# Kernel optimization log

Hardware: AMD Instinct MI355X
Metric: run time of the kernel (lower is better)

Reference implementation:

```python
import jax, jax.numpy as jnp
import numpy as np

D = 2048; Nl = 2; Nh = 32; Nkv = 8; V = 32000; Dh = 5632; Lm = 4096
B = 1; L = 2048; E = 1e-5
DHEAD = D // Nh  # 64


def setup_inputs() -> dict:
    key = jax.random.key(0)
    ks = jax.random.split(key, 10)
    s = 0.02
    rn = lambda k, shape: jax.random.normal(k, shape, jnp.float32) * s
    emb = rn(ks[0], (V, D))
    wq = rn(ks[1], (Nl, D, D))
    wk = rn(ks[2], (Nl, D, D * Nkv // Nh))
    wv = rn(ks[3], (Nl, D, D * Nkv // Nh))
    wa = rn(ks[4], (Nl, D, D))
    wg = rn(ks[5], (Nl, D, Dh))
    wu = rn(ks[6], (Nl, D, Dh))
    wd = rn(ks[7], (Nl, Dh, D))
    w_an = jnp.ones((Nl, D), jnp.float32)
    w_fn = jnp.ones((Nl, D), jnp.float32)
    w_on = jnp.ones((D,), jnp.float32)
    w_out = rn(ks[8], (D, V))
    # RoPE tables (interleaved-pair convention, matching reshape(..., -1, 2))
    theta = 1.0 / (10000.0 ** (jnp.arange(0, DHEAD, 2, dtype=jnp.float32) / DHEAD))
    freqs = jnp.outer(jnp.arange(Lm, dtype=jnp.float32), theta)  # [Lm, DHEAD//2]
    cos = jnp.cos(freqs)
    sin = jnp.sin(freqs)
    ti = jax.random.randint(ks[9], (B, L), 0, V)
    return dict(ti=ti, emb=emb, wq=wq, wk=wk, wv=wv, wa=wa, w_an=w_an, w_fn=w_fn,
                wg=wg, wu=wu, wd=wd, w_on=w_on, w_out=w_out, cos=cos, sin=sin)


def _rmsnorm(x, w):
    return x * jax.lax.rsqrt(jnp.mean(x * x, -1, keepdims=True) + E) * w


def _rope(x, cos, sin):
    # x: [B, L, H, DHEAD]; cos/sin: [1, L, 1, DHEAD//2]; interleaved pairs
    xs = x.reshape(*x.shape[:-1], DHEAD // 2, 2)
    xr, xi = xs[..., 0], xs[..., 1]
    r1 = xr * cos - xi * sin
    i1 = xr * sin + xi * cos
    return jnp.stack([r1, i1], axis=-1).reshape(x.shape)


def reference(ti, emb, wq, wk, wv, wa, w_an, w_fn, wg, wu, wd, w_on, w_out, cos, sin):
    cos_l = cos[:L].reshape(1, L, 1, DHEAD // 2)
    sin_l = sin[:L].reshape(1, L, 1, DHEAD // 2)
    mask = jnp.triu(jnp.full((1, 1, L, L), -jnp.inf, jnp.float32), 1)
    scale = 1.0 / jnp.sqrt(jnp.float32(DHEAD))
    rep = Nh // Nkv
    x = emb[ti]  # [B, L, D]
    for l in range(Nl):
        h = _rmsnorm(x, w_an[l])
        q = (h @ wq[l]).reshape(B, L, Nh, DHEAD)
        k = (h @ wk[l]).reshape(B, L, Nkv, DHEAD)
        v = (h @ wv[l]).reshape(B, L, Nkv, DHEAD)
        q = _rope(q, cos_l, sin_l)
        k = _rope(k, cos_l, sin_l)
        kx = jnp.repeat(k, rep, axis=2)  # GQA expand -> [B, L, Nh, DHEAD]
        vx = jnp.repeat(v, rep, axis=2)
        a = jnp.einsum('blhd,bmhd->bhlm', q, kx) * scale
        p = jax.nn.softmax(a + mask, axis=-1)
        sa = jnp.einsum('bhlm,bmhd->blhd', p, vx).reshape(B, L, D)
        x = x + sa @ wa[l]
        hf = _rmsnorm(x, w_fn[l])
        x = x + (jax.nn.silu(hf @ wg[l]) * (hf @ wu[l])) @ wd[l]
    return _rmsnorm(x, w_on) @ w_out  # [B, L, V]
```

## Files before the change

### kernel.cpp

```cpp
#include <hip/hip_runtime.h>
#include <hip/hip_bf16.h>

#define DMODEL 2048
#define LSEQ   2048
#define NHEAD  32
#define NKVH   8
#define DHEAD  64
#define DFF    5632
#define VOCAB  32000

typedef __attribute__((ext_vector_type(8))) short bf16x8;
typedef __attribute__((ext_vector_type(4))) float f32x4;
typedef __attribute__((ext_vector_type(8))) unsigned short ushort8;

__device__ __forceinline__ void gload_lds16(const __hip_bfloat16* g, __hip_bfloat16* l) {
  __builtin_amdgcn_global_load_lds((const void __attribute__((address_space(1)))*)g,
                                   (void __attribute__((address_space(3)))*)l, 16, 0, 0);
}

__device__ __forceinline__ float bfbits2f(unsigned short u) {
  return __uint_as_float(((unsigned int)u) << 16);
}
__device__ __forceinline__ unsigned short f2bfbits(float f) {
  unsigned int x = __float_as_uint(f);
  return (unsigned short)((x + 0x7fffu + ((x >> 16) & 1u)) >> 16);
}

__global__ __launch_bounds__(256) void embed_k(const int* __restrict__ ti,
                                               const float* __restrict__ emb,
                                               float* __restrict__ x) {
  const int row = blockIdx.x;
  const int t = threadIdx.x;
  const int tok = ti[row];
  const float4* s = (const float4*)(emb + (size_t)tok * DMODEL);
  float4* d = (float4*)(x + (size_t)row * DMODEL);
  d[t] = s[t];
  d[t + 256] = s[t + 256];
}

__global__ __launch_bounds__(256) void rmsnorm_k(const float* __restrict__ x,
                                                 const float* __restrict__ w,
                                                 __hip_bfloat16* __restrict__ out) {
  const int row = blockIdx.x;
  const int t = threadIdx.x;
  const float4* xr = (const float4*)(x + (size_t)row * DMODEL);
  float4 a = xr[t];
  float4 b = xr[t + 256];
  float ss = a.x*a.x + a.y*a.y + a.z*a.z + a.w*a.w
           + b.x*b.x + b.y*b.y + b.z*b.z + b.w*b.w;
  #pragma unroll
  for (int m = 32; m >= 1; m >>= 1) ss += __shfl_xor(ss, m);
  __shared__ float red[4];
  if ((t & 63) == 0) red[t >> 6] = ss;
  __syncthreads();
  const float tot = red[0] + red[1] + red[2] + red[3];
  const float sc = rsqrtf(tot * (1.0f / DMODEL) + 1e-5f);
  const float4* w4 = (const float4*)w;
  float4 wa_ = w4[t], wb_ = w4[t + 256];
  __hip_bfloat16* o = out + (size_t)row * DMODEL;
  o[4*t + 0] = __float2bfloat16(a.x * sc * wa_.x);
  o[4*t + 1] = __float2bfloat16(a.y * sc * wa_.y);
  o[4*t + 2] = __float2bfloat16(a.z * sc * wa_.z);
  o[4*t + 3] = __float2bfloat16(a.w * sc * wa_.w);
  o[1024 + 4*t + 0] = __float2bfloat16(b.x * sc * wb_.x);
  o[1024 + 4*t + 1] = __float2bfloat16(b.y * sc * wb_.y);
  o[1024 + 4*t + 2] = __float2bfloat16(b.z * sc * wb_.z);
  o[1024 + 4*t + 3] = __float2bfloat16(b.w * sc * wb_.w);
}

__global__ __launch_bounds__(256) void transpose_k(const float* __restrict__ src,
                                                   __hip_bfloat16* __restrict__ dst,
                                                   int K, int N, int rstride, int roff) {
  __shared__ float tile[64 * 65];
  const int kb = blockIdx.x * 64;
  const int nb = blockIdx.y * 64;
  const int t = threadIdx.x;
  #pragma unroll
  for (int i = 0; i < 16; ++i) {
    const int idx = t + 256 * i;
    const int r = idx >> 6, c = idx & 63;
    tile[r * 65 + c] = src[(size_t)(kb + r) * N + nb + c];
  }
  __syncthreads();
  #pragma unroll
  for (int i = 0; i < 16; ++i) {
    const int idx = t + 256 * i;
    const int n = idx >> 6, k = idx & 63;
    dst[((size_t)(nb + n) * rstride + roff) * K + kb + k] = __float2bfloat16(tile[k * 65 + n]);
  }
}

template <int EPI>
__global__ __launch_bounds__(256) void gemm_bt(const __hip_bfloat16* __restrict__ A,
                                               const __hip_bfloat16* __restrict__ Bt,
                                               float* __restrict__ Cf,
                                               __hip_bfloat16* __restrict__ Cb,
                                               int M, int N, int K) {
  __shared__ __align__(16) __hip_bfloat16 As[128 * 32];
  __shared__ __align__(16) __hip_bfloat16 Bs[128 * 32];
  const int tid = threadIdx.x;
  const int wave = tid >> 6;
  const int lane = tid & 63;
  const int nbx = M >> 7;
  const int nwg = nbx * (N >> 7);
  const int orig = blockIdx.y * nbx + blockIdx.x;
  const int wid = (orig & 7) * (nwg >> 3) + (orig >> 3);
  const int tm = (wid % nbx) << 7;
  const int tn = (wid / nbx) << 7;
  const int wr = (wave >> 1) * 64;
  const int wc = (wave & 1) * 64;
  const int fr = lane & 15;
  const int fg = lane >> 4;
  const f32x4 fzero = {0.f, 0.f, 0.f, 0.f};
  f32x4 acc[4][4];
  #pragma unroll
  for (int i = 0; i < 4; ++i)
    #pragma unroll
    for (int j = 0; j < 4; ++j) acc[i][j] = fzero;
  const int srow = wave * 32 + (lane >> 2);
  const int scol = (lane & 3) * 8;
  const __hip_bfloat16* gA = A + (size_t)(tm + srow) * K + scol;
  const __hip_bfloat16* gB = Bt + (size_t)(tn + srow) * K + scol;
  __hip_bfloat16* lA = &As[wave * 1024];
  __hip_bfloat16* lB = &Bs[wave * 1024];
  for (int k0 = 0; k0 < K; k0 += 32) {
    gload_lds16(gA, lA);
    gload_lds16(gA + (size_t)16 * K, lA + 512);
    gload_lds16(gB, lB);
    gload_lds16(gB + (size_t)16 * K, lB + 512);
    gA += 32; gB += 32;
    __syncthreads();
    bf16x8 af[4], bfr[4];
    #pragma unroll
    for (int i = 0; i < 4; ++i) af[i] = *(const bf16x8*)&As[(wr + i * 16 + fr) * 32 + fg * 8];
    #pragma unroll
    for (int j = 0; j < 4; ++j) bfr[j] = *(const bf16x8*)&Bs[(wc + j * 16 + fr) * 32 + fg * 8];
    #pragma unroll
    for (int i = 0; i < 4; ++i)
      #pragma unroll
      for (int j = 0; j < 4; ++j)
        acc[i][j] = __builtin_amdgcn_mfma_f32_16x16x32_bf16(af[i], bfr[j], acc[i][j], 0, 0, 0);
    __syncthreads();
  }
  #pragma unroll
  for (int i = 0; i < 4; ++i)
    #pragma unroll
    for (int j = 0; j < 4; ++j)
      #pragma unroll
      for (int r = 0; r < 4; ++r) {
        const int row = tm + wr + i * 16 + fg * 4 + r;
        const int col = tn + wc + j * 16 + fr;
        const float v = acc[i][j][r];
        if (EPI == 0) Cf[(size_t)row * N + col] = v;
        else if (EPI == 1) Cb[(size_t)row * N + col] = __float2bfloat16(v);
        else Cf[(size_t)row * N + col] += v;
      }
}

template <int EPI>
__global__ __launch_bounds__(512, 2) void gemm8p(const __hip_bfloat16* __restrict__ A,
                                                 const __hip_bfloat16* __restrict__ Bt,
                                                 float* __restrict__ Cf,
                                                 __hip_bfloat16* __restrict__ Cb,
                                                 int M, int N, int K) {
  __shared__ __align__(16) __hip_bfloat16 lds[2][2][256 * 64];
  const int tid = threadIdx.x;
  const int wave = tid >> 6;
  const int lane = tid & 63;
  const int nbx = M >> 8;
  const int nwg = nbx * (N >> 8);
  const int orig = blockIdx.y * nbx + blockIdx.x;
  const int wid = (orig & 7) * (nwg >> 3) + (orig >> 3);
  const int tm = (wid % nbx) << 8;
  const int tn = (wid / nbx) << 8;
  const int wm = wave >> 2;
  const int wn = wave & 3;
  const int fr = lane & 15;
  const int fg = lane >> 4;
  const int l3 = lane >> 3;
  const int l7 = lane & 7;
  const int swzcol = (l3 ^ l7) << 3;
  const size_t sK = (size_t)K;

  const __hip_bfloat16* pA = A + (size_t)(tm + wave * 8 + l3) * sK + swzcol;
  const __hip_bfloat16* pB = Bt + (size_t)(tn + wave * 8 + l3) * sK + swzcol;

  #pragma unroll
  for (int j = 0; j < 4; ++j) {
    gload_lds16(pA + (size_t)(j * 64) * sK, &lds[0][0][(j * 64 + wave * 8) * 64]);
    gload_lds16(pB + (size_t)(j * 64) * sK, &lds[0][1][(j * 64 + wave * 8) * 64]);
  }
  pA += 64; pB += 64;
  #pragma unroll
  for (int j = 0; j < 4; ++j) {
    gload_lds16(pA + (size_t)(j * 64) * sK, &lds[1][0][(j * 64 + wave * 8) * 64]);
    gload_lds16(pB + (size_t)(j * 64) * sK, &lds[1][1][(j * 64 + wave * 8) * 64]);
  }
  pA += 64; pB += 64;

  const f32x4 fzero = {0.f, 0.f, 0.f, 0.f};
  f32x4 acc[8][4];
  #pragma unroll
  for (int i = 0; i < 8; ++i)
    #pragma unroll
    for (int j = 0; j < 4; ++j) acc[i][j] = fzero;

  const int wmo = wm * 128;
  const int wno = wn * 64;
  const int rswz = (fr & 7) << 4;
  const int ct0 = ((fg * 16) ^ rswz) >> 1;
  const int ct1 = ((64 + fg * 16) ^ rswz) >> 1;

  asm volatile("s_waitcnt vmcnt(8)" ::: "memory");
  __builtin_amdgcn_s_barrier();
  __builtin_amdgcn_sched_barrier(0);

  const int NT = K >> 6;
  for (int kt = 0; kt < NT; ++kt) {
    const int cur = kt & 1;
    const __hip_bfloat16* LA = &lds[cur][0][0];
    const __hip_bfloat16* LB = &lds[cur][1][0];
    bf16x8 av[8][2], bv[4][2];
    #pragma unroll
    for (int mi = 0; mi < 8; ++mi) {
      av[mi][0] = *(const bf16x8*)&LA[(wmo + mi * 16 + fr) * 64 + ct0];
      av[mi][1] = *(const bf16x8*)&LA[(wmo + mi * 16 + fr) * 64 + ct1];
    }
    #pragma unroll
    for (int ni = 0; ni < 4; ++ni) {
      bv[ni][0] = *(const bf16x8*)&LB[(wno + ni * 16 + fr) * 64 + ct0];
      bv[ni][1] = *(const bf16x8*)&LB[(wno + ni * 16 + fr) * 64 + ct1];
    }
    asm volatile("s_waitcnt lgkmcnt(0)" ::: "memory");
    __builtin_amdgcn_sched_barrier(0);
    __builtin_amdgcn_s_barrier();
    __builtin_amdgcn_sched_barrier(0);
    const bool pre = (kt + 2 < NT);
    #pragma unroll
    for (int q = 0; q < 4; ++q) {
      if (pre) {
        gload_lds16(pA + (size_t)(q * 64) * sK, &lds[cur][0][(q * 64 + wave * 8) * 64]);
        gload_lds16(pB + (size_t)(q * 64) * sK, &lds[cur][1][(q * 64 + wave * 8) * 64]);
      }
      const int mb = (q & 1) * 4;
      const int nb = (q >> 1) * 2;
      __builtin_amdgcn_s_setprio(1);
      #pragma unroll
      for (int mi = 0; mi < 4; ++mi)
        #pragma unroll
        for (int ni = 0; ni < 2; ++ni) {
          acc[mb + mi][nb + ni] = __builtin_amdgcn_mfma_f32_16x16x32_bf16(
              av[mb + mi][0], bv[nb + ni][0], acc[mb + mi][nb + ni], 0, 0, 0);
          acc[mb + mi][nb + ni] = __builtin_amdgcn_mfma_f32_16x16x32_bf16(
              av[mb + mi][1], bv[nb + ni][1], acc[mb + mi][nb + ni], 0, 0, 0);
        }
      __builtin_amdgcn_s_setprio(0);
    }
    if (pre) { pA += 64; pB += 64; }
    if (kt + 1 < NT) {
      if (pre) asm volatile("s_waitcnt vmcnt(8)" ::: "memory");
      else     asm volatile("s_waitcnt vmcnt(0)" ::: "memory");
      __builtin_amdgcn_s_barrier();
      __builtin_amdgcn_sched_barrier(0);
    }
  }
  #pragma unroll
  for (int mf = 0; mf < 8; ++mf)
    #pragma unroll
    for (int nf = 0; nf < 4; ++nf)
      #pragma unroll
      for (int r = 0; r < 4; ++r) {
        const int row = tm + wmo + mf * 16 + fg * 4 + r;
        const int col = tn + wno + nf * 16 + fr;
        const float v = acc[mf][nf][r];
        if (EPI == 0) Cf[(size_t)row * N + col] = v;
        else if (EPI == 1) Cb[(size_t)row * N + col] = __float2bfloat16(v);
        else if (EPI == 3) {
          const float p = __shfl_xor(v, 1);
          if (!(fr & 1)) {
            const float sv = v / (1.f + __expf(-v)) * p;
            Cb[(size_t)row * (N >> 1) + ((tn + wno + nf * 16) >> 1) + (fr >> 1)] =
                __float2bfloat16(sv);
          }
        }
      }
}

__global__ __launch_bounds__(256) void rope_k(__hip_bfloat16* __restrict__ qkv,
                                              const float* __restrict__ cosT,
                                              const float* __restrict__ sinT) {
  const int row = blockIdx.x;
  const int t = threadIdx.x;
  unsigned int* base = (unsigned int*)(qkv + (size_t)row * 3072);
  #pragma unroll
  for (int p = t; p < 1280; p += 256) {
    const int hp = p >> 5;
    const int i = p & 31;
    const unsigned int packed = base[hp * 32 + i];
    const float x0 = bfbits2f((unsigned short)(packed & 0xffffu));
    const float x1 = bfbits2f((unsigned short)(packed >> 16));
    const float c = cosT[row * 32 + i];
    const float s = sinT[row * 32 + i];
    const float r0 = x0 * c - x1 * s;
    const float r1 = x0 * s + x1 * c;
    base[hp * 32 + i] = (unsigned int)f2bfbits(r0) | ((unsigned int)f2bfbits(r1) << 16);
  }
}

__global__ __launch_bounds__(256) void attn_k(const __hip_bfloat16* __restrict__ qkv,
                                              __hip_bfloat16* __restrict__ out) {
  const int h = blockIdx.x;
  const int qt = blockIdx.y;
  const int tid = threadIdx.x;
  const int wave = tid >> 6;
  const int lane = tid & 63;
  const int fr = lane & 15;
  const int fg = lane >> 4;
  const int qb = qt * 64;
  const int kcol = DMODEL + (h >> 2) * DHEAD;
  const int vcol = DMODEL + NKVH * DHEAD + (h >> 2) * DHEAD;
  __shared__ __align__(16) __hip_bfloat16 Ks[64 * 64];
  __shared__ __align__(16) __hip_bfloat16 Vt[64 * 72];
  __shared__ __align__(16) __hip_bfloat16 Ps[4][16 * 72];
  bf16x8 qf[2];
  {
    const __hip_bfloat16* qp = qkv + (size_t)(qb + wave * 16 + fr) * 3072 + h * DHEAD + fg * 8;
    qf[0] = *(const bf16x8*)qp;
    qf[1] = *(const bf16x8*)(qp + 32);
  }
  const f32x4 fzero = {0.f, 0.f, 0.f, 0.f};
  float m_run = -1e30f, l_run = 0.f;
  f32x4 o[4];
  #pragma unroll
  for (int c = 0; c < 4; ++c) o[c] = fzero;

  const int kr8 = lane >> 3;
  const int kgr = ((lane & 7) ^ kr8) << 3;
  const int vpr = tid >> 3;
  const int vg = tid & 7;
  const int myq = qb + wave * 16 + fr;
  const int fr7 = fr & 7;

  for (int t = 0; t <= qt; ++t) {
    {
      const __hip_bfloat16* kp = qkv + (size_t)(t * 64 + wave * 16 + kr8) * 3072 + kcol + kgr;
      gload_lds16(kp, &Ks[(wave * 16) * 64]);
      gload_lds16(kp + (size_t)8 * 3072, &Ks[(wave * 16 + 8) * 64]);
    }
    {
      const __hip_bfloat16* vp0 = qkv + (size_t)(t * 64 + 2 * vpr) * 3072 + vcol + vg * 8;
      ushort8 va = *(const ushort8*)vp0;
      ushort8 vb = *(const ushort8*)(vp0 + 3072);
      unsigned short* vt = (unsigned short*)Vt;
      #pragma unroll
      for (int i = 0; i < 8; ++i) {
        unsigned int pk = (unsigned int)va[i] | ((unsigned int)vb[i] << 16);
        *(unsigned int*)(vt + (vg * 8 + i) * 72 + 2 * vpr) = pk;
      }
    }
    __syncthreads();
    f32x4 s[4];
    #pragma unroll
    for (int c = 0; c < 4; ++c) {
      s[c] = fzero;
      #pragma unroll
      for (int ks = 0; ks < 2; ++ks) {
        bf16x8 kf = *(const bf16x8*)&Ks[(c * 16 + fr) * 64 + (((ks * 4 + fg) ^ fr7) << 3)];
        s[c] = __builtin_amdgcn_mfma_f32_16x16x32_bf16(kf, qf[ks], s[c], 0, 0, 0);
      }
    }
    float pm = -1e30f;
    #pragma unroll
    for (int c = 0; c < 4; ++c)
      #pragma unroll
      for (int r = 0; r < 4; ++r) {
        float v = s[c][r] * 0.125f;
        if (t * 64 + c * 16 + fg * 4 + r > myq) v = -1e30f;
        s[c][r] = v;
        pm = fmaxf(pm, v);
      }
    pm = fmaxf(pm, __shfl_xor(pm, 16));
    pm = fmaxf(pm, __shfl_xor(pm, 32));
    const float mn = fmaxf(m_run, pm);
    const float al = __expf(m_run - mn);
    m_run = mn;
    float rs = 0.f;
    #pragma unroll
    for (int c = 0; c < 4; ++c)
      #pragma unroll
      for (int r = 0; r < 4; ++r) {
        float p = __expf(s[c][r] - mn);
        s[c][r] = p;
        rs += p;
      }
    rs += __shfl_xor(rs, 16);
    rs += __shfl_xor(rs, 32);
    l_run = l_run * al + rs;
    float als[4];
    #pragma unroll
    for (int r = 0; r < 4; ++r) als[r] = __shfl(al, fg * 4 + r);
    #pragma unroll
    for (int c = 0; c < 4; ++c)
      #pragma unroll
      for (int r = 0; r < 4; ++r) o[c][r] *= als[r];
    {
      unsigned short* pw = (unsigned short*)Ps[wave];
      #pragma unroll
      for (int c = 0; c < 4; ++c) {
        unsigned int lo = (unsigned int)f2bfbits(s[c][0]) | ((unsigned int)f2bfbits(s[c][1]) << 16);
        unsigned int hi = (unsigned int)f2bfbits(s[c][2]) | ((unsigned int)f2bfbits(s[c][3]) << 16);
        uint2 pk; pk.x = lo; pk.y = hi;
        *(uint2*)(pw + fr * 72 + c * 16 + fg * 4) = pk;
      }
    }
    #pragma unroll
    for (int ks = 0; ks < 2; ++ks) {
      bf16x8 pf = *(const bf16x8*)&Ps[wave][fr * 72 + ks * 32 + fg * 8];
      #pragma unroll
      for (int c = 0; c < 4; ++c) {
        bf16x8 vf = *(const bf16x8*)&Vt[(c * 16 + fr) * 72 + ks * 32 + fg * 8];
        o[c] = __builtin_amdgcn_mfma_f32_16x16x32_bf16(pf, vf, o[c], 0, 0, 0);
      }
    }
    __syncthreads();
  }
  float lq[4];
  #pragma unroll
  for (int r = 0; r < 4; ++r) lq[r] = __shfl(l_run, fg * 4 + r);
  #pragma unroll
  for (int c = 0; c < 4; ++c)
    #pragma unroll
    for (int r = 0; r < 4; ++r)
      out[(size_t)(qb + wave * 16 + fg * 4 + r) * DMODEL + h * DHEAD + c * 16 + fr] =
          __float2bfloat16(o[c][r] / lq[r]);
}

extern "C" void kernel_launch(void* const* d_in, const int* in_sizes, int n_in,
                              void* d_out, int out_size, void* d_ws, size_t ws_size,
                              hipStream_t stream) {
  const int* ti = (const int*)d_in[0];
  const float* emb = (const float*)d_in[1];
  const float* wq = (const float*)d_in[2];
  const float* wk = (const float*)d_in[3];
  const float* wv = (const float*)d_in[4];
  const float* wa = (const float*)d_in[5];
  const float* w_an = (const float*)d_in[6];
  const float* w_fn = (const float*)d_in[7];
  const float* wg = (const float*)d_in[8];
  const float* wu = (const float*)d_in[9];
  const float* wd = (const float*)d_in[10];
  const float* w_on = (const float*)d_in[11];
  const float* w_out = (const float*)d_in[12];
  const float* cosT = (const float*)d_in[13];
  const float* sinT = (const float*)d_in[14];
  float* outp = (float*)d_out;

  char* ws = (char*)d_ws;
  float* x            = (float*)(ws + 0);
  __hip_bfloat16* h   = (__hip_bfloat16*)(ws + 16777216);
  __hip_bfloat16* qkv = (__hip_bfloat16*)(ws + 25165824);
  __hip_bfloat16* att = (__hip_bfloat16*)(ws + 37748736);
  __hip_bfloat16* mb  = (__hip_bfloat16*)(ws + 92274688);
  __hip_bfloat16* wTqkv = (__hip_bfloat16*)(ws + 115343360);
  __hip_bfloat16* wTa   = (__hip_bfloat16*)(ws + 127926272);
  __hip_bfloat16* wTgu  = (__hip_bfloat16*)(ws + 136314880);
  __hip_bfloat16* wTd   = (__hip_bfloat16*)(ws + 182452224);
  __hip_bfloat16* wTout = (__hip_bfloat16*)(ws + 25165824);
  (void)in_sizes; (void)n_in; (void)out_size; (void)ws_size;

  const dim3 blk(256);
  embed_k<<<2048, blk, 0, stream>>>(ti, emb, x);
  for (int l = 0; l < 2; ++l) {
    transpose_k<<<dim3(32, 32), blk, 0, stream>>>(wq + (size_t)l * 2048 * 2048, wTqkv, 2048, 2048, 1, 0);
    transpose_k<<<dim3(32, 8),  blk, 0, stream>>>(wk + (size_t)l * 2048 * 512, wTqkv + (size_t)2048 * 2048, 2048, 512, 1, 0);
    transpose_k<<<dim3(32, 8),  blk, 0, stream>>>(wv + (size_t)l * 2048 * 512, wTqkv + (size_t)2560 * 2048, 2048, 512, 1, 0);
    transpose_k<<<dim3(32, 32), blk, 0, stream>>>(wa + (size_t)l * 2048 * 2048, wTa, 2048, 2048, 1, 0);
    transpose_k<<<dim3(32, 88), blk, 0, stream>>>(wg + (size_t)l * 2048 * 5632, wTgu, 2048, 5632, 2, 0);
    transpose_k<<<dim3(32, 88), blk, 0, stream>>>(wu + (size_t)l * 2048 * 5632, wTgu, 2048, 5632, 2, 1);
    transpose_k<<<dim3(88, 32), blk, 0, stream>>>(wd + (size_t)l * 5632 * 2048, wTd, 5632, 2048, 1, 0);

    rmsnorm_k<<<2048, blk, 0, stream>>>(x, w_an + l * 2048, h);
    gemm_bt<1><<<dim3(16, 24), blk, 0, stream>>>(h, wTqkv, nullptr, qkv, 2048, 3072, 2048);
    rope_k<<<2048, blk, 0, stream>>>(qkv, cosT, sinT);
    attn_k<<<dim3(32, 32), blk, 0, stream>>>(qkv, att);
    gemm_bt<2><<<dim3(16, 16), blk, 0, stream>>>(att, wTa, x, nullptr, 2048, 2048, 2048);

    rmsnorm_k<<<2048, blk, 0, stream>>>(x, w_fn + l * 2048, h);
    gemm8p<3><<<dim3(8, 44), dim3(512), 0, stream>>>(h, wTgu, nullptr, mb, 2048, 11264, 2048);
    gemm_bt<2><<<dim3(16, 16), blk, 0, stream>>>(mb, wTd, x, nullptr, 2048, 2048, 5632);
  }
  transpose_k<<<dim3(32, 500), blk, 0, stream>>>(w_out, wTout, 2048, 32000, 1, 0);
  rmsnorm_k<<<2048, blk, 0, stream>>>(x, w_on, h);
  gemm8p<0><<<dim3(8, 125), dim3(512), 0, stream>>>(h, wTout, outp, nullptr, 2048, 32000, 2048);
}
```

Baseline: 1.424 ms.

## Double GEMM K-tile to 64 with XOR-swizzled LDS layout

Raises the bf16 GEMM K step per iteration from 32 to 64, halving the number of barrier pairs and loop iterations per tile. It also XOR-swizzles the 16-byte chunk positions in LDS, both when loading from global and when reading fragments, to avoid LDS bank conflicts on the 128-byte row stride. The cost is more LDS per block and more fragment registers, which could lower occupancy.

After: 1.344 ms. 1.06x faster.

```diff
diff --git a/kernel.cpp b/kernel.cpp
--- a/kernel.cpp
+++ b/kernel.cpp
@@ -96,8 +96,8 @@
                                                float* __restrict__ Cf,
                                                __hip_bfloat16* __restrict__ Cb,
                                                int M, int N, int K) {
-  __shared__ __align__(16) __hip_bfloat16 As[128 * 32];
-  __shared__ __align__(16) __hip_bfloat16 Bs[128 * 32];
+  __shared__ __align__(16) __hip_bfloat16 As[128 * 64];
+  __shared__ __align__(16) __hip_bfloat16 Bs[128 * 64];
   const int tid = threadIdx.x;
   const int wave = tid >> 6;
   const int lane = tid & 63;
@@ -111,35 +111,45 @@
   const int wc = (wave & 1) * 64;
   const int fr = lane & 15;
   const int fg = lane >> 4;
+  const int r8 = lane >> 3;
+  const int gsrc = ((lane & 7) ^ r8) << 3;
+  const int fr7 = fr & 7;
   const f32x4 fzero = {0.f, 0.f, 0.f, 0.f};
   f32x4 acc[4][4];
   #pragma unroll
   for (int i = 0; i < 4; ++i)
     #pragma unroll
     for (int j = 0; j < 4; ++j) acc[i][j] = fzero;
-  const int srow = wave * 32 + (lane >> 2);
-  const int scol = (lane & 3) * 8;
-  const __hip_bfloat16* gA = A + (size_t)(tm + srow) * K + scol;
-  const __hip_bfloat16* gB = Bt + (size_t)(tn + srow) * K + scol;
-  __hip_bfloat16* lA = &As[wave * 1024];
-  __hip_bfloat16* lB = &Bs[wave * 1024];
-  for (int k0 = 0; k0 < K; k0 += 32) {
-    gload_lds16(gA, lA);
-    gload_lds16(gA + (size_t)16 * K, lA + 512);
-    gload_lds16(gB, lB);
-    gload_lds16(gB + (size_t)16 * K, lB + 512);
-    gA += 32; gB += 32;
+  const __hip_bfloat16* gA = A + (size_t)(tm + wave * 32 + r8) * K + gsrc;
+  const __hip_bfloat16* gB = Bt + (size_t)(tn + wave * 32 + r8) * K + gsrc;
+  const int c0 = ((0 + fg) ^ fr7) << 3;
+  const int c1 = ((4 + fg) ^ fr7) << 3;
+  for (int k0 = 0; k0 < K; k0 += 64) {
+    #pragma unroll
+    for (int j = 0; j < 4; ++j) {
+      gload_lds16(gA + (size_t)(j * 8) * K, &As[(wave * 32 + j * 8) * 64]);
+      gload_lds16(gB + (size_t)(j * 8) * K, &Bs[(wave * 32 + j * 8) * 64]);
+    }
+    gA += 64; gB += 64;
     __syncthreads();
-    bf16x8 af[4], bfr[4];
-    #pragma unroll
-    for (int i = 0; i < 4; ++i) af[i] = *(const bf16x8*)&As[(wr + i * 16 + fr) * 32 + fg * 8];
-    #pragma unroll
-    for (int j = 0; j < 4; ++j) bfr[j] = *(const bf16x8*)&Bs[(wc + j * 16 + fr) * 32 + fg * 8];
+    bf16x8 af[4][2], bfr[4][2];
+    #pragma unroll
+    for (int i = 0; i < 4; ++i) {
+      af[i][0] = *(const bf16x8*)&As[(wr + i * 16 + fr) * 64 + c0];
+      af[i][1] = *(const bf16x8*)&As[(wr + i * 16 + fr) * 64 + c1];
+    }
+    #pragma unroll
+    for (int j = 0; j < 4; ++j) {
+      bfr[j][0] = *(const bf16x8*)&Bs[(wc + j * 16 + fr) * 64 + c0];
+      bfr[j][1] = *(const bf16x8*)&Bs[(wc + j * 16 + fr) * 64 + c1];
+    }
     #pragma unroll
     for (int i = 0; i < 4; ++i)
       #pragma unroll
-      for (int j = 0; j < 4; ++j)
-        acc[i][j] = __builtin_amdgcn_mfma_f32_16x16x32_bf16(af[i], bfr[j], acc[i][j], 0, 0, 0);
+      for (int j = 0; j < 4; ++j) {
+        acc[i][j] = __builtin_amdgcn_mfma_f32_16x16x32_bf16(af[i][0], bfr[j][0], acc[i][j], 0, 0, 0);
+        acc[i][j] = __builtin_amdgcn_mfma_f32_16x16x32_bf16(af[i][1], bfr[j][1], acc[i][j], 0, 0, 0);
+      }
     __syncthreads();
   }
   #pragma unroll
```
